# Kernel optimization log

Measured on AMD Instinct MI355X. Metric: run time of the kernel, lower is better.

The kernel has to match this reference:

```python
import jax, jax.numpy as jnp
import numpy as np

N = 50000      # nodes
F = 128        # feature_dim
H = 128        # hidden_dim
E = 1_600_000  # edges
G = 64         # graphs in batch
A = 8          # n_actions


def setup_inputs() -> dict:
    key = jax.random.key(0)
    ks = jax.random.split(key, 12)
    s = 0.05
    return {
        "x": jax.random.normal(ks[0], (N, F), jnp.float32),
        "edge_attr": jax.random.uniform(ks[1], (E, 1), jnp.float32),
        "W_e1": jax.random.normal(ks[2], (3, 1), jnp.float32) * s,
        "b_e1": jnp.zeros((1,), jnp.float32),
        "W_e2": jax.random.normal(ks[3], (1, 1), jnp.float32) * s,
        "b_e2": jnp.zeros((1,), jnp.float32),
        "W_gcn": jax.random.normal(ks[4], (F, H), jnp.float32) * s,
        "b_gcn": jnp.zeros((H,), jnp.float32),
        "W2": jax.random.normal(ks[5], (H, H), jnp.float32) * s,
        "b2": jnp.zeros((H,), jnp.float32),
        "W3": jax.random.normal(ks[6], (H, A), jnp.float32) * s,
        "b3": jnp.zeros((A,), jnp.float32),
        "edge_index": jax.random.randint(ks[7], (2, E), 0, N, jnp.int64),
        "batch": jnp.sort(jax.random.randint(ks[8], (N,), 0, G, jnp.int64)),
    }


def reference(x, edge_attr, W_e1, b_e1, W_e2, b_e2, W_gcn, b_gcn, W2, b2, W3, b3, edge_index, batch):
    # edge MLP: input is [src, dst, edge_attr] per edge -> (E, 3)
    e_feat = jnp.concatenate([edge_index.T.astype(x.dtype), edge_attr], axis=1)
    h = jax.nn.relu(e_feat @ W_e1 + b_e1)
    w = jax.nn.sigmoid(h @ W_e2 + b_e2)[:, 0]  # (E,)

    # GCNConv: add self-loops (weight 1), symmetric normalization
    loop = jnp.arange(N)
    row = jnp.concatenate([edge_index[0], loop])      # source
    col = jnp.concatenate([edge_index[1], loop])      # target
    w_all = jnp.concatenate([w, jnp.ones((N,), w.dtype)])
    deg = jax.ops.segment_sum(w_all, col, num_segments=N)
    safe_deg = jnp.where(deg > 0, deg, 1.0)
    dis = jnp.where(deg > 0, 1.0 / jnp.sqrt(safe_deg), 0.0)  # deg^-1/2, inf->0
    norm = dis[row] * w_all * dis[col]                # (E+N,)

    xw = x @ W_gcn                                    # (N, H)
    msg = norm[:, None] * xw[row]                     # (E+N, H) gather
    conv = jax.ops.segment_sum(msg, col, num_segments=N) + b_gcn  # scatter
    h1 = jax.nn.relu(conv)

    # global_mean_pool over batch index
    sums = jax.ops.segment_sum(h1, batch, num_segments=G)
    cnt = jax.ops.segment_sum(jnp.ones((N,), h1.dtype), batch, num_segments=G)
    pooled = sums / jnp.maximum(cnt, 1.0)[:, None]    # (G, H)

    h2 = jax.nn.relu(pooled @ W2 + b2)
    return h2 @ W3 + b3                               # (G, A)
```

## Files before the change

### kernel.cpp

```cpp
#include <hip/hip_runtime.h>
#include <hip/hip_fp16.h>
#include <math.h>

#define GB 64
#define AD 8
#define NC2 256
#define BSH 6
#define BS  64
#define NBMAX 1024

typedef _Float16 half8 __attribute__((ext_vector_type(8)));
typedef float    f32x4 __attribute__((ext_vector_type(4)));

__global__ __launch_bounds__(512) void k_hist2(const int* __restrict__ ei,
                                               int* __restrict__ H2,
                                               int E, int ce, int NB) {
    __shared__ int h[NBMAX];
    int c = blockIdx.x;
    for (int b = threadIdx.x; b < NB; b += 512) h[b] = 0;
    __syncthreads();
    int e0 = c * ce, e1 = min(e0 + ce, E);
    int nv = (e1 - e0) & ~3;
    const int4* dst4 = (const int4*)(ei + E + e0);
    for (int v = threadIdx.x; v < (nv >> 2); v += 512) {
        int4 d = dst4[v];
        atomicAdd(&h[d.x >> BSH], 1);
        atomicAdd(&h[d.y >> BSH], 1);
        atomicAdd(&h[d.z >> BSH], 1);
        atomicAdd(&h[d.w >> BSH], 1);
    }
    for (int e = e0 + nv + threadIdx.x; e < e1; e += 512)
        atomicAdd(&h[ei[E + e] >> BSH], 1);
    __syncthreads();
    for (int b = threadIdx.x; b < NB; b += 512)
        H2[(size_t)c * NB + b] = h[b];
}

__global__ __launch_bounds__(256) void k_cscan(int* __restrict__ H2,
                                               int* __restrict__ cntB,
                                               int NB, int nc) {
    __shared__ int ssum[256];
    int b = blockIdx.x;
    int t = threadIdx.x;
    int v = (t < nc) ? H2[(size_t)t * NB + b] : 0;
    ssum[t] = v;
    __syncthreads();
    for (int s = 1; s < 256; s <<= 1) {
        int tmp = (t >= s) ? ssum[t - s] : 0;
        __syncthreads();
        ssum[t] += tmp;
        __syncthreads();
    }
    if (t < nc) H2[(size_t)t * NB + b] = ssum[t] - v;
    if (t == 255) cntB[b] = ssum[255];
}

__global__ __launch_bounds__(1024) void k_bscan(const int* __restrict__ cntB,
                                                int* __restrict__ bb,
                                                int* __restrict__ rowptr,
                                                float* __restrict__ psum,
                                                int NB, int n, int E) {
    __shared__ int sm[1024];
    int t = threadIdx.x;
    for (int z = t; z < GB * 128 + GB; z += 1024) psum[z] = 0.0f;
    int v = (t < NB) ? cntB[t] : 0;
    sm[t] = v;
    __syncthreads();
    for (int s = 1; s < 1024; s <<= 1) {
        int tmp = (t >= s) ? sm[t - s] : 0;
        __syncthreads();
        sm[t] += tmp;
        __syncthreads();
    }
    if (t < NB) bb[t] = sm[t] - v;
    if (t == NB - 1) bb[NB] = sm[t];
    if (t == 0) rowptr[n] = E;
}

__global__ __launch_bounds__(512) void k_fill2(const int* __restrict__ ei,
                                               const float* __restrict__ attr,
                                               const float* __restrict__ W_e1,
                                               const float* __restrict__ b_e1,
                                               const float* __restrict__ W_e2,
                                               const float* __restrict__ b_e2,
                                               const int* __restrict__ bb,
                                               const int* __restrict__ H2,
                                               int2* __restrict__ rec,
                                               int E, int ce, int NB) {
    __shared__ int off[NBMAX];
    int c = blockIdx.x;
    for (int b = threadIdx.x; b < NB; b += 512)
        off[b] = bb[b] + H2[(size_t)c * NB + b];
    __syncthreads();
    float w1s = W_e1[0], w1d = W_e1[1], w1a = W_e1[2], bb1 = b_e1[0];
    float w2 = W_e2[0], bb2 = b_e2[0];
    int e0 = c * ce, e1 = min(e0 + ce, E);
    int nv = (e1 - e0) & ~3;
    const int4*   src4 = (const int4*)(ei + e0);
    const int4*   dst4 = (const int4*)(ei + E + e0);
    const float4* att4 = (const float4*)(attr + e0);
    for (int v = threadIdx.x; v < (nv >> 2); v += 512) {
        int4 sv = src4[v];
        int4 dv = dst4[v];
        float4 av = att4[v];
        int   ss[4] = {sv.x, sv.y, sv.z, sv.w};
        int   dd[4] = {dv.x, dv.y, dv.z, dv.w};
        float aa[4] = {av.x, av.y, av.z, av.w};
        #pragma unroll
        for (int k = 0; k < 4; k++) {
            float h = fmaxf((float)ss[k] * w1s + (float)dd[k] * w1d + aa[k] * w1a + bb1, 0.0f);
            float w = 1.0f / (1.0f + expf(-(h * w2 + bb2)));
            int pos = atomicAdd(&off[dd[k] >> BSH], 1);
            int2 rv;
            rv.x = ss[k] | ((dd[k] & (BS - 1)) << 16);
            rv.y = __float_as_int(w);
            rec[pos] = rv;
        }
    }
    for (int e = e0 + nv + threadIdx.x; e < e1; e += 512) {
        int d = ei[E + e];
        int s = ei[e];
        float h = fmaxf((float)s * w1s + (float)d * w1d + attr[e] * w1a + bb1, 0.0f);
        float w = 1.0f / (1.0f + expf(-(h * w2 + bb2)));
        int pos = atomicAdd(&off[d >> BSH], 1);
        int2 rv;
        rv.x = s | ((d & (BS - 1)) << 16);
        rv.y = __float_as_int(w);
        rec[pos] = rv;
    }
}

__global__ __launch_bounds__(256) void k_bucket(const int2* __restrict__ rec,
                                                const int* __restrict__ bb,
                                                unsigned int* __restrict__ rec3,
                                                int* __restrict__ rowptr,
                                                float* __restrict__ dis, int n) {
    __shared__ int   cntL[BS];
    __shared__ float degL[BS];
    __shared__ int   pfx[BS];
    __shared__ int   cnt2[BS];
    int b = blockIdx.x;
    int t = threadIdx.x;
    if (t < BS) { cntL[t] = 0; degL[t] = 1.0f; cnt2[t] = 0; }
    __syncthreads();
    int s0 = bb[b], s1 = bb[b + 1];
    for (int j = s0 + t; j < s1; j += 256) {
        int2 rv = rec[j];
        int dl = (rv.x >> 16) & (BS - 1);
        atomicAdd(&cntL[dl], 1);
        atomicAdd(&degL[dl], __int_as_float(rv.y));
    }
    __syncthreads();
    if (t == 0) {
        int acc = 0;
        for (int k = 0; k < BS; k++) { pfx[k] = acc; acc += cntL[k]; }
    }
    __syncthreads();
    int lo = b << BSH;
    if (t < BS) {
        int i = lo + t;
        if (i < n) {
            rowptr[i] = s0 + pfx[t];
            dis[i] = rsqrtf(degL[t]);
        }
    }
    for (int j = s0 + t; j < s1; j += 256) {
        int2 rv = rec[j];
        int dl = (rv.x >> 16) & (BS - 1);
        int r = atomicAdd(&cnt2[dl], 1);
        unsigned int hh = (unsigned int)__half_as_ushort(
                              __float2half(__int_as_float(rv.y)));
        rec3[s0 + pfx[dl] + r] = (unsigned int)(rv.x & 0xFFFF) | (hh << 16);
    }
}

__global__ __launch_bounds__(256) void k_xw(const float* __restrict__ x,
                                            const float* __restrict__ Wg,
                                            const float* __restrict__ dis,
                                            __half* __restrict__ xwh, int n) {
    __shared__ _Float16 Wh[128 * 136];
    int tid = threadIdx.x;
    for (int idx = tid; idx < 128 * 128; idx += 256) {
        int k = idx >> 7, c = idx & 127;
        Wh[c * 136 + k] = (_Float16)Wg[idx];
    }
    __syncthreads();

    int lane = tid & 63;
    int w = tid >> 6;
    int n16 = lane & 15;
    int quad = lane >> 4;

    #pragma unroll
    for (int hf = 0; hf < 2; hf++) {
        int r0 = blockIdx.x * 128 + hf * 64 + w * 16;
        if (r0 >= n) break;
        int arow = min(r0 + n16, n - 1);
        const float* xrow = x + (size_t)arow * 128;

        f32x4 acc[8];
        #pragma unroll
        for (int nt = 0; nt < 8; nt++) acc[nt] = (f32x4){0.f, 0.f, 0.f, 0.f};

        #pragma unroll
        for (int kk = 0; kk < 4; kk++) {
            int k0 = kk * 32 + quad * 8;
            float4 f0 = *(const float4*)(xrow + k0);
            float4 f1 = *(const float4*)(xrow + k0 + 4);
            half8 a;
            a[0] = (_Float16)f0.x; a[1] = (_Float16)f0.y;
            a[2] = (_Float16)f0.z; a[3] = (_Float16)f0.w;
            a[4] = (_Float16)f1.x; a[5] = (_Float16)f1.y;
            a[6] = (_Float16)f1.z; a[7] = (_Float16)f1.w;
            #pragma unroll
            for (int nt = 0; nt < 8; nt++) {
                half8 b = *(const half8*)&Wh[(nt * 16 + n16) * 136 + k0];
                acc[nt] = __builtin_amdgcn_mfma_f32_16x16x32_f16(a, b, acc[nt], 0, 0, 0);
            }
        }

        #pragma unroll
        for (int r = 0; r < 4; r++) {
            int row = r0 + quad * 4 + r;
            if (row < n) {
                float dv = dis[row];
                #pragma unroll
                for (int nt = 0; nt < 8; nt++)
                    xwh[(size_t)row * 128 + nt * 16 + n16] = __float2half(acc[nt][r] * dv);
            }
        }
    }
}

__global__ __launch_bounds__(256) void k_gather(const unsigned int* __restrict__ rec3,
                                                const int* __restrict__ rowptr,
                                                const float* __restrict__ dis,
                                                const __half* __restrict__ xh,
                                                const float* __restrict__ bg,
                                                __half* __restrict__ conv, int n) {
    int wave = threadIdx.x >> 6;
    int lane = threadIdx.x & 63;
    int g = lane >> 4;
    int q = lane & 15;
    int i = blockIdx.x * 4 + wave;
    if (i >= n) return;
    int st = rowptr[i];
    int m = rowptr[i + 1] - st;
    float di = dis[i];
    float acc[8];
    {
        uint4 sr = *(const uint4*)(xh + (size_t)i * 128 + q * 8);
        const __half2* hp = (const __half2*)&sr;
        float sc = (g == 0) ? 1.0f : 0.0f;
        #pragma unroll
        for (int k = 0; k < 4; k++) {
            float2 f = __half22float2(hp[k]);
            acc[2 * k]     = sc * f.x;
            acc[2 * k + 1] = sc * f.y;
        }
    }
    for (int base = 0; base < m; base += 64) {
        int kk = min(64, m - base);
        unsigned int rv = 0u;
        if (lane < kk) rv = rec3[st + base + lane];
        int jn = (kk + 3) >> 2;
        #pragma unroll 8
        for (int j = 0; j < jn; j++) {
            unsigned int rvj = (unsigned int)__builtin_amdgcn_ds_bpermute(
                                   ((j << 2) + g) << 2, (int)rv);
            int s = rvj & 0xFFFF;
            float cf = __half2float(__ushort_as_half((unsigned short)(rvj >> 16)));
            uint4 rw = *(const uint4*)(xh + (size_t)s * 128 + q * 8);
            const __half2* rp = (const __half2*)&rw;
            #pragma unroll
            for (int k = 0; k < 4; k++) {
                float2 f = __half22float2(rp[k]);
                acc[2 * k]     += cf * f.x;
                acc[2 * k + 1] += cf * f.y;
            }
        }
    }
    #pragma unroll
    for (int k = 0; k < 8; k++) {
        acc[k] += __shfl_xor(acc[k], 16);
        acc[k] += __shfl_xor(acc[k], 32);
    }
    if (g == 0) {
        float4 b0 = *(const float4*)(bg + q * 8);
        float4 b1 = *(const float4*)(bg + q * 8 + 4);
        const float* bp = (const float*)&b0;
        float v[8];
        #pragma unroll
        for (int k = 0; k < 4; k++) v[k] = fmaxf(di * acc[k] + bp[k], 0.0f);
        bp = (const float*)&b1;
        #pragma unroll
        for (int k = 0; k < 4; k++) v[4 + k] = fmaxf(di * acc[4 + k] + bp[k], 0.0f);
        __half2 h[4];
        #pragma unroll
        for (int k = 0; k < 4; k++)
            h[k] = __halves2half2(__float2half(v[2 * k]), __float2half(v[2 * k + 1]));
        uint4 o;
        o.x = *(unsigned int*)&h[0];
        o.y = *(unsigned int*)&h[1];
        o.z = *(unsigned int*)&h[2];
        o.w = *(unsigned int*)&h[3];
        *(uint4*)(conv + (size_t)i * 128 + q * 8) = o;
    }
}

__device__ __forceinline__ int lbound(const int* __restrict__ a, int n, int v) {
    int lo = 0, hi = n;
    while (lo < hi) {
        int mid = (lo + hi) >> 1;
        if (a[mid] < v) lo = mid + 1; else hi = mid;
    }
    return lo;
}

__global__ __launch_bounds__(256) void k_pool(const __half* __restrict__ h1,
                                              const int* __restrict__ batch,
                                              float* __restrict__ psum,
                                              float* __restrict__ pcnt, int n) {
    int g = blockIdx.x, ch = blockIdx.y;
    int t = threadIdx.x;
    int s = lbound(batch, n, g);
    int e = lbound(batch, n, g + 1);
    int rq = t >> 6, q = t & 63;
    float ax = 0.0f, ay = 0.0f;
    for (int i = s + ch * 4 + rq; i < e; i += 16) {
        __half2 hv = *(const __half2*)(h1 + (size_t)i * 128 + 2 * q);
        float2 f = __half22float2(hv);
        ax += f.x; ay += f.y;
    }
    __shared__ float2 sm[256];
    sm[t] = make_float2(ax, ay);
    __syncthreads();
    if (t < 64) {
        float2 a0 = sm[t], a1 = sm[t + 64], a2 = sm[t + 128], a3 = sm[t + 192];
        atomicAdd(&psum[g * 128 + 2 * q],     a0.x + a1.x + a2.x + a3.x);
        atomicAdd(&psum[g * 128 + 2 * q + 1], a0.y + a1.y + a2.y + a3.y);
    }
    if (ch == 0 && t == 0) pcnt[g] = (float)(e - s);
}

__global__ __launch_bounds__(128) void k_head(const float* __restrict__ psum,
                                              const float* __restrict__ pcnt,
                                              const float* __restrict__ W2,
                                              const float* __restrict__ b2,
                                              const float* __restrict__ W3,
                                              const float* __restrict__ b3,
                                              float* __restrict__ out) {
    __shared__ float pl[128];
    __shared__ float h2s[128];
    int g = blockIdx.x;
    int t = threadIdx.x;
    float c = fmaxf(pcnt[g], 1.0f);
    pl[t] = psum[g * 128 + t] / c;
    __syncthreads();
    float acc = b2[t];
    for (int k = 0; k < 128; k++) acc += pl[k] * W2[k * 128 + t];
    h2s[t] = fmaxf(acc, 0.0f);
    __syncthreads();
    if (t < AD) {
        float o = b3[t];
        for (int k = 0; k < 128; k++) o += h2s[k] * W3[k * AD + t];
        out[g * AD + t] = o;
    }
}

extern "C" void kernel_launch(void* const* d_in, const int* in_sizes, int n_in,
                              void* d_out, int out_size, void* d_ws, size_t ws_size,
                              hipStream_t stream) {
    const float* x        = (const float*)d_in[0];
    const float* edge_attr= (const float*)d_in[1];
    const float* W_e1     = (const float*)d_in[2];
    const float* b_e1     = (const float*)d_in[3];
    const float* W_e2     = (const float*)d_in[4];
    const float* b_e2     = (const float*)d_in[5];
    const float* W_gcn    = (const float*)d_in[6];
    const float* b_gcn    = (const float*)d_in[7];
    const float* W2       = (const float*)d_in[8];
    const float* b2       = (const float*)d_in[9];
    const float* W3       = (const float*)d_in[10];
    const float* b3       = (const float*)d_in[11];
    const int*   ei       = (const int*)d_in[12];
    const int*   batch    = (const int*)d_in[13];
    float* out = (float*)d_out;

    const int E  = in_sizes[12] / 2;
    const int n  = in_sizes[13];
    const int NB = (n + BS - 1) >> BSH;
    const int ce = (((E + NC2 - 1) / NC2) + 3) & ~3;

    char* p = (char*)d_ws;
    __half* xwh   = (__half*)p;  p += (size_t)n * 128 * sizeof(__half);
    int*    H2    = (int*)p;
    __half* conv  = (__half*)p;  p += (size_t)n * 128 * sizeof(__half);
    int2*   rec   = (int2*)p;    p += (size_t)E * sizeof(int2);
    unsigned int* rec3 = (unsigned int*)p; p += (size_t)E * sizeof(unsigned int);
    float*  dis   = (float*)p;   p += (size_t)n * sizeof(float);
    float*  psum  = (float*)p;   p += (size_t)GB * 128 * sizeof(float);
    float*  pcnt  = (float*)p;   p += (size_t)GB * sizeof(float);
    int*    rowptr= (int*)p;     p += (size_t)(n + 1) * sizeof(int);
    int*    cntB  = (int*)p;     p += (size_t)NBMAX * sizeof(int);
    int*    bb    = (int*)p;     p += (size_t)(NBMAX + 1) * sizeof(int);

    k_hist2<<<NC2, 512, 0, stream>>>(ei, H2, E, ce, NB);
    k_cscan<<<NB, 256, 0, stream>>>(H2, cntB, NB, NC2);
    k_bscan<<<1, 1024, 0, stream>>>(cntB, bb, rowptr, psum, NB, n, E);
    k_fill2<<<NC2, 512, 0, stream>>>(ei, edge_attr, W_e1, b_e1, W_e2, b_e2,
                                     bb, H2, rec, E, ce, NB);
    k_bucket<<<NB, 256, 0, stream>>>(rec, bb, rec3, rowptr, dis, n);
    k_xw<<<(n + 127) / 128, 256, 0, stream>>>(x, W_gcn, dis, xwh, n);
    k_gather<<<(n + 3) / 4, 256, 0, stream>>>(rec3, rowptr, dis, xwh,
                                              b_gcn, conv, n);
    k_pool<<<dim3(GB, 4), 256, 0, stream>>>(conv, batch, psum, pcnt, n);
    k_head<<<GB, 128, 0, stream>>>(psum, pcnt, W2, b2, W3, b3, out);
}
```

Baseline: 235.3 us.

## Split xw into four 32-feature planes and gather one plane per grid slice

After: 295.6 us. +25.6%, slower.

```diff
diff --git a/kernel.cpp b/kernel.cpp
--- a/kernel.cpp
+++ b/kernel.cpp
@@ -11,6 +11,7 @@
 
 typedef _Float16 half8 __attribute__((ext_vector_type(8)));
 typedef float    f32x4 __attribute__((ext_vector_type(4)));
+typedef unsigned int u32x4 __attribute__((ext_vector_type(4)));
 
 __global__ __launch_bounds__(512) void k_hist2(const int* __restrict__ ei,
                                                int* __restrict__ H2,
@@ -177,7 +178,7 @@
 __global__ __launch_bounds__(256) void k_xw(const float* __restrict__ x,
                                             const float* __restrict__ Wg,
                                             const float* __restrict__ dis,
-                                            __half* __restrict__ xwh, int n) {
+                                            __half* __restrict__ xwp, int n) {
     __shared__ _Float16 Wh[128 * 136];
     int tid = threadIdx.x;
     for (int idx = tid; idx < 128 * 128; idx += 256) {
@@ -225,8 +226,11 @@
             if (row < n) {
                 float dv = dis[row];
                 #pragma unroll
-                for (int nt = 0; nt < 8; nt++)
-                    xwh[(size_t)row * 128 + nt * 16 + n16] = __float2half(acc[nt][r] * dv);
+                for (int nt = 0; nt < 8; nt++) {
+                    int c = nt * 16 + n16;
+                    xwp[(size_t)(c >> 5) * n * 32 + (size_t)row * 32 + (c & 31)] =
+                        __float2half(acc[nt][r] * dv);
+                }
             }
         }
     }
@@ -235,21 +239,23 @@
 __global__ __launch_bounds__(256) void k_gather(const unsigned int* __restrict__ rec3,
                                                 const int* __restrict__ rowptr,
                                                 const float* __restrict__ dis,
-                                                const __half* __restrict__ xh,
+                                                const __half* __restrict__ xwp,
                                                 const float* __restrict__ bg,
                                                 __half* __restrict__ conv, int n) {
     int wave = threadIdx.x >> 6;
     int lane = threadIdx.x & 63;
-    int g = lane >> 4;
-    int q = lane & 15;
+    int g = lane >> 2;
+    int q = lane & 3;
+    int p = blockIdx.y;
     int i = blockIdx.x * 4 + wave;
     if (i >= n) return;
+    const __half* plane = xwp + (size_t)p * n * 32;
     int st = rowptr[i];
     int m = rowptr[i + 1] - st;
     float di = dis[i];
     float acc[8];
     {
-        uint4 sr = *(const uint4*)(xh + (size_t)i * 128 + q * 8);
+        u32x4 sr = *(const u32x4*)(plane + (size_t)i * 32 + q * 8);
         const __half2* hp = (const __half2*)&sr;
         float sc = (g == 0) ? 1.0f : 0.0f;
         #pragma unroll
@@ -262,15 +268,16 @@
     for (int base = 0; base < m; base += 64) {
         int kk = min(64, m - base);
         unsigned int rv = 0u;
-        if (lane < kk) rv = rec3[st + base + lane];
-        int jn = (kk + 3) >> 2;
-        #pragma unroll 8
+        if (lane < kk)
+            rv = __builtin_nontemporal_load(rec3 + st + base + lane);
+        int jn = (kk + 15) >> 4;
+        #pragma unroll 4
         for (int j = 0; j < jn; j++) {
             unsigned int rvj = (unsigned int)__builtin_amdgcn_ds_bpermute(
-                                   ((j << 2) + g) << 2, (int)rv);
+                                   ((j << 4) + g) << 2, (int)rv);
             int s = rvj & 0xFFFF;
             float cf = __half2float(__ushort_as_half((unsigned short)(rvj >> 16)));
-            uint4 rw = *(const uint4*)(xh + (size_t)s * 128 + q * 8);
+            u32x4 rw = *(const u32x4*)(plane + (size_t)s * 32 + q * 8);
             const __half2* rp = (const __half2*)&rw;
             #pragma unroll
             for (int k = 0; k < 4; k++) {
@@ -282,12 +289,15 @@
     }
     #pragma unroll
     for (int k = 0; k < 8; k++) {
+        acc[k] += __shfl_xor(acc[k], 4);
+        acc[k] += __shfl_xor(acc[k], 8);
         acc[k] += __shfl_xor(acc[k], 16);
         acc[k] += __shfl_xor(acc[k], 32);
     }
     if (g == 0) {
-        float4 b0 = *(const float4*)(bg + q * 8);
-        float4 b1 = *(const float4*)(bg + q * 8 + 4);
+        int f0 = p * 32 + q * 8;
+        float4 b0 = *(const float4*)(bg + f0);
+        float4 b1 = *(const float4*)(bg + f0 + 4);
         const float* bp = (const float*)&b0;
         float v[8];
         #pragma unroll
@@ -299,12 +309,12 @@
         #pragma unroll
         for (int k = 0; k < 4; k++)
             h[k] = __halves2half2(__float2half(v[2 * k]), __float2half(v[2 * k + 1]));
-        uint4 o;
+        u32x4 o;
         o.x = *(unsigned int*)&h[0];
         o.y = *(unsigned int*)&h[1];
         o.z = *(unsigned int*)&h[2];
         o.w = *(unsigned int*)&h[3];
-        *(uint4*)(conv + (size_t)i * 128 + q * 8) = o;
+        __builtin_nontemporal_store(o, (u32x4*)(conv + (size_t)i * 128 + f0));
     }
 }
 
@@ -393,7 +403,7 @@
     const int ce = (((E + NC2 - 1) / NC2) + 3) & ~3;
 
     char* p = (char*)d_ws;
-    __half* xwh   = (__half*)p;  p += (size_t)n * 128 * sizeof(__half);
+    __half* xwp   = (__half*)p;  p += (size_t)n * 128 * sizeof(__half);
     int*    H2    = (int*)p;
     __half* conv  = (__half*)p;  p += (size_t)n * 128 * sizeof(__half);
     int2*   rec   = (int2*)p;    p += (size_t)E * sizeof(int2);
@@ -411,9 +421,9 @@
     k_fill2<<<NC2, 512, 0, stream>>>(ei, edge_attr, W_e1, b_e1, W_e2, b_e2,
                                      bb, H2, rec, E, ce, NB);
     k_bucket<<<NB, 256, 0, stream>>>(rec, bb, rec3, rowptr, dis, n);
-    k_xw<<<(n + 127) / 128, 256, 0, stream>>>(x, W_gcn, dis, xwh, n);
-    k_gather<<<(n + 3) / 4, 256, 0, stream>>>(rec3, rowptr, dis, xwh,
-                                              b_gcn, conv, n);
+    k_xw<<<(n + 127) / 128, 256, 0, stream>>>(x, W_gcn, dis, xwp, n);
+    k_gather<<<dim3((n + 3) / 4, 4), 256, 0, stream>>>(rec3, rowptr, dis, xwp,
+                                                       b_gcn, conv, n);
     k_pool<<<dim3(GB, 4), 256, 0, stream>>>(conv, batch, psum, pcnt, n);
     k_head<<<GB, 128, 0, stream>>>(psum, pcnt, W2, b2, W3, b3, out);
 }
```

## Stage bucket records in LDS and use nontemporal loads/stores in gather

Applied to the files above, without the earlier changes.

Measured after the change: 237.2 us. Within noise of the previous version (+0.8%).

```diff
diff --git a/kernel.cpp b/kernel.cpp
--- a/kernel.cpp
+++ b/kernel.cpp
@@ -8,9 +8,11 @@
 #define BSH 6
 #define BS  64
 #define NBMAX 1024
+#define CAP 3072
 
 typedef _Float16 half8 __attribute__((ext_vector_type(8)));
 typedef float    f32x4 __attribute__((ext_vector_type(4)));
+typedef unsigned int u32x4 __attribute__((ext_vector_type(4)));
 
 __global__ __launch_bounds__(512) void k_hist2(const int* __restrict__ ei,
                                                int* __restrict__ H2,
@@ -135,6 +137,8 @@
                                                 unsigned int* __restrict__ rec3,
                                                 int* __restrict__ rowptr,
                                                 float* __restrict__ dis, int n) {
+    __shared__ int2  sr[CAP];
+    __shared__ unsigned int outp[CAP];
     __shared__ int   cntL[BS];
     __shared__ float degL[BS];
     __shared__ int   pfx[BS];
@@ -144,33 +148,69 @@
     if (t < BS) { cntL[t] = 0; degL[t] = 1.0f; cnt2[t] = 0; }
     __syncthreads();
     int s0 = bb[b], s1 = bb[b + 1];
-    for (int j = s0 + t; j < s1; j += 256) {
-        int2 rv = rec[j];
-        int dl = (rv.x >> 16) & (BS - 1);
-        atomicAdd(&cntL[dl], 1);
-        atomicAdd(&degL[dl], __int_as_float(rv.y));
-    }
-    __syncthreads();
-    if (t == 0) {
-        int acc = 0;
-        for (int k = 0; k < BS; k++) { pfx[k] = acc; acc += cntL[k]; }
-    }
-    __syncthreads();
-    int lo = b << BSH;
-    if (t < BS) {
-        int i = lo + t;
-        if (i < n) {
-            rowptr[i] = s0 + pfx[t];
-            dis[i] = rsqrtf(degL[t]);
-        }
-    }
-    for (int j = s0 + t; j < s1; j += 256) {
-        int2 rv = rec[j];
-        int dl = (rv.x >> 16) & (BS - 1);
-        int r = atomicAdd(&cnt2[dl], 1);
-        unsigned int hh = (unsigned int)__half_as_ushort(
-                              __float2half(__int_as_float(rv.y)));
-        rec3[s0 + pfx[dl] + r] = (unsigned int)(rv.x & 0xFFFF) | (hh << 16);
+    int m = s1 - s0;
+    if (m <= CAP) {
+        for (int j = t; j < m; j += 256) {
+            int2 rv = rec[s0 + j];
+            sr[j] = rv;
+            int dl = (rv.x >> 16) & (BS - 1);
+            atomicAdd(&cntL[dl], 1);
+            atomicAdd(&degL[dl], __int_as_float(rv.y));
+        }
+        __syncthreads();
+        if (t == 0) {
+            int acc = 0;
+            for (int k = 0; k < BS; k++) { pfx[k] = acc; acc += cntL[k]; }
+        }
+        __syncthreads();
+        int lo = b << BSH;
+        if (t < BS) {
+            int i = lo + t;
+            if (i < n) {
+                rowptr[i] = s0 + pfx[t];
+                dis[i] = rsqrtf(degL[t]);
+            }
+        }
+        for (int j = t; j < m; j += 256) {
+            int2 rv = sr[j];
+            int dl = (rv.x >> 16) & (BS - 1);
+            int r = atomicAdd(&cnt2[dl], 1);
+            unsigned int hh = (unsigned int)__half_as_ushort(
+                                  __float2half(__int_as_float(rv.y)));
+            outp[pfx[dl] + r] = (unsigned int)(rv.x & 0xFFFF) | (hh << 16);
+        }
+        __syncthreads();
+        for (int j = t; j < m; j += 256)
+            rec3[s0 + j] = outp[j];
+    } else {
+        for (int j = s0 + t; j < s1; j += 256) {
+            int2 rv = rec[j];
+            int dl = (rv.x >> 16) & (BS - 1);
+            atomicAdd(&cntL[dl], 1);
+            atomicAdd(&degL[dl], __int_as_float(rv.y));
+        }
+        __syncthreads();
+        if (t == 0) {
+            int acc = 0;
+            for (int k = 0; k < BS; k++) { pfx[k] = acc; acc += cntL[k]; }
+        }
+        __syncthreads();
+        int lo = b << BSH;
+        if (t < BS) {
+            int i = lo + t;
+            if (i < n) {
+                rowptr[i] = s0 + pfx[t];
+                dis[i] = rsqrtf(degL[t]);
+            }
+        }
+        for (int j = s0 + t; j < s1; j += 256) {
+            int2 rv = rec[j];
+            int dl = (rv.x >> 16) & (BS - 1);
+            int r = atomicAdd(&cnt2[dl], 1);
+            unsigned int hh = (unsigned int)__half_as_ushort(
+                                  __float2half(__int_as_float(rv.y)));
+            rec3[s0 + pfx[dl] + r] = (unsigned int)(rv.x & 0xFFFF) | (hh << 16);
+        }
     }
 }
 
@@ -249,7 +289,7 @@
     float di = dis[i];
     float acc[8];
     {
-        uint4 sr = *(const uint4*)(xh + (size_t)i * 128 + q * 8);
+        u32x4 sr = *(const u32x4*)(xh + (size_t)i * 128 + q * 8);
         const __half2* hp = (const __half2*)&sr;
         float sc = (g == 0) ? 1.0f : 0.0f;
         #pragma unroll
@@ -262,7 +302,8 @@
     for (int base = 0; base < m; base += 64) {
         int kk = min(64, m - base);
         unsigned int rv = 0u;
-        if (lane < kk) rv = rec3[st + base + lane];
+        if (lane < kk)
+            rv = __builtin_nontemporal_load(rec3 + st + base + lane);
         int jn = (kk + 3) >> 2;
         #pragma unroll 8
         for (int j = 0; j < jn; j++) {
@@ -270,7 +311,7 @@
                                    ((j << 2) + g) << 2, (int)rv);
             int s = rvj & 0xFFFF;
             float cf = __half2float(__ushort_as_half((unsigned short)(rvj >> 16)));
-            uint4 rw = *(const uint4*)(xh + (size_t)s * 128 + q * 8);
+            u32x4 rw = *(const u32x4*)(xh + (size_t)s * 128 + q * 8);
             const __half2* rp = (const __half2*)&rw;
             #pragma unroll
             for (int k = 0; k < 4; k++) {
@@ -299,12 +340,12 @@
         #pragma unroll
         for (int k = 0; k < 4; k++)
             h[k] = __halves2half2(__float2half(v[2 * k]), __float2half(v[2 * k + 1]));
-        uint4 o;
+        u32x4 o;
         o.x = *(unsigned int*)&h[0];
         o.y = *(unsigned int*)&h[1];
         o.z = *(unsigned int*)&h[2];
         o.w = *(unsigned int*)&h[3];
-        *(uint4*)(conv + (size_t)i * 128 + q * 8) = o;
+        __builtin_nontemporal_store(o, (u32x4*)(conv + (size_t)i * 128 + q * 8));
     }
 }
 
```

## Fuse bucket-local sort, gather and mean-pool into one per-bucket kernel

Applied to the files above, without the earlier changes.

Result: slower. 253.3 us (+7.7%).

```diff
diff --git a/kernel.cpp b/kernel.cpp
--- a/kernel.cpp
+++ b/kernel.cpp
@@ -8,9 +8,12 @@
 #define BSH 6
 #define BS  64
 #define NBMAX 1024
+#define CAP 3072
+#define GSPAN 4
 
 typedef _Float16 half8 __attribute__((ext_vector_type(8)));
 typedef float    f32x4 __attribute__((ext_vector_type(4)));
+typedef unsigned int u32x4 __attribute__((ext_vector_type(4)));
 
 __global__ __launch_bounds__(512) void k_hist2(const int* __restrict__ ei,
                                                int* __restrict__ H2,
@@ -62,7 +65,7 @@
                                                 int NB, int n, int E) {
     __shared__ int sm[1024];
     int t = threadIdx.x;
-    for (int z = t; z < GB * 128 + GB; z += 1024) psum[z] = 0.0f;
+    for (int z = t; z < GB * 128; z += 1024) psum[z] = 0.0f;
     int v = (t < NB) ? cntB[t] : 0;
     sm[t] = v;
     __syncthreads();
@@ -130,18 +133,16 @@
     }
 }
 
-__global__ __launch_bounds__(256) void k_bucket(const int2* __restrict__ rec,
-                                                const int* __restrict__ bb,
-                                                unsigned int* __restrict__ rec3,
-                                                int* __restrict__ rowptr,
-                                                float* __restrict__ dis, int n) {
+__global__ __launch_bounds__(256) void k_deg(const int2* __restrict__ rec,
+                                             const int* __restrict__ bb,
+                                             int* __restrict__ rowptr,
+                                             float* __restrict__ dis, int n) {
     __shared__ int   cntL[BS];
     __shared__ float degL[BS];
     __shared__ int   pfx[BS];
-    __shared__ int   cnt2[BS];
     int b = blockIdx.x;
     int t = threadIdx.x;
-    if (t < BS) { cntL[t] = 0; degL[t] = 1.0f; cnt2[t] = 0; }
+    if (t < BS) { cntL[t] = 0; degL[t] = 1.0f; }
     __syncthreads();
     int s0 = bb[b], s1 = bb[b + 1];
     for (int j = s0 + t; j < s1; j += 256) {
@@ -163,14 +164,6 @@
             rowptr[i] = s0 + pfx[t];
             dis[i] = rsqrtf(degL[t]);
         }
-    }
-    for (int j = s0 + t; j < s1; j += 256) {
-        int2 rv = rec[j];
-        int dl = (rv.x >> 16) & (BS - 1);
-        int r = atomicAdd(&cnt2[dl], 1);
-        unsigned int hh = (unsigned int)__half_as_ushort(
-                              __float2half(__int_as_float(rv.y)));
-        rec3[s0 + pfx[dl] + r] = (unsigned int)(rv.x & 0xFFFF) | (hh << 16);
     }
 }
 
@@ -232,79 +225,135 @@
     }
 }
 
-__global__ __launch_bounds__(256) void k_gather(const unsigned int* __restrict__ rec3,
+__global__ __launch_bounds__(512) void k_gather(const int2* __restrict__ rec,
+                                                const int* __restrict__ bb,
                                                 const int* __restrict__ rowptr,
                                                 const float* __restrict__ dis,
+                                                const int* __restrict__ batch,
                                                 const __half* __restrict__ xh,
                                                 const float* __restrict__ bg,
-                                                __half* __restrict__ conv, int n) {
-    int wave = threadIdx.x >> 6;
-    int lane = threadIdx.x & 63;
+                                                float* __restrict__ psum, int n) {
+    __shared__ unsigned int outL[CAP];
+    __shared__ float psumL[GSPAN * 128];
+    __shared__ int   rowL[BS];
+    __shared__ int   cntL[BS];
+    __shared__ int   batchL[BS];
+    __shared__ float disL[BS];
+    int b = blockIdx.x;
+    int t = threadIdx.x;
+    int lo = b << BSH;
+    int s0 = bb[b], s1 = bb[b + 1];
+    int m_all = s1 - s0;
+    if (t < GSPAN * 128) psumL[t] = 0.0f;
+    if (t < BS) {
+        int i = lo + t;
+        cntL[t] = 0;
+        if (i < n) {
+            rowL[t] = rowptr[i] - s0;
+            batchL[t] = batch[i];
+            disL[t] = dis[i];
+        } else {
+            rowL[t] = m_all; batchL[t] = -1; disL[t] = 0.0f;
+        }
+    }
+    __syncthreads();
+    int gb0 = batchL[0];
+    int hiN = min(lo + BS - 1, n - 1);
+    int span = batch[hiN] - gb0 + 1;
+
+    bool fast = (m_all <= CAP);
+    if (fast) {
+        for (int j = t; j < m_all; j += 512) {
+            int2 rv = rec[s0 + j];
+            int dl = (rv.x >> 16) & (BS - 1);
+            int r = atomicAdd(&cntL[dl], 1);
+            unsigned int hh = (unsigned int)__half_as_ushort(
+                                  __float2half(__int_as_float(rv.y)));
+            outL[rowL[dl] + r] = (unsigned int)(rv.x & 0xFFFF) | (hh << 16);
+        }
+    }
+    __syncthreads();
+
+    int wave = t >> 6;
+    int lane = t & 63;
     int g = lane >> 4;
     int q = lane & 15;
-    int i = blockIdx.x * 4 + wave;
-    if (i >= n) return;
-    int st = rowptr[i];
-    int m = rowptr[i + 1] - st;
-    float di = dis[i];
-    float acc[8];
-    {
-        uint4 sr = *(const uint4*)(xh + (size_t)i * 128 + q * 8);
-        const __half2* hp = (const __half2*)&sr;
-        float sc = (g == 0) ? 1.0f : 0.0f;
+    for (int k = 0; k < 8; k++) {
+        int dl = wave * 8 + k;
+        int i = lo + dl;
+        if (i >= n) break;
+        int st = rowL[dl];
+        int m = cntL[dl];
+        float di = disL[dl];
+        float acc[8];
+        {
+            u32x4 sr = *(const u32x4*)(xh + (size_t)i * 128 + q * 8);
+            const __half2* hp = (const __half2*)&sr;
+            float sc = (g == 0) ? 1.0f : 0.0f;
+            #pragma unroll
+            for (int kk = 0; kk < 4; kk++) {
+                float2 f = __half22float2(hp[kk]);
+                acc[2 * kk]     = sc * f.x;
+                acc[2 * kk + 1] = sc * f.y;
+            }
+        }
+        if (fast) {
+            #pragma unroll 4
+            for (int j = g; j < m; j += 4) {
+                unsigned int u = outL[st + j];
+                int s = u & 0xFFFF;
+                float cf = __half2float(__ushort_as_half((unsigned short)(u >> 16)));
+                u32x4 rw = *(const u32x4*)(xh + (size_t)s * 128 + q * 8);
+                const __half2* rp = (const __half2*)&rw;
+                #pragma unroll
+                for (int kk = 0; kk < 4; kk++) {
+                    float2 f = __half22float2(rp[kk]);
+                    acc[2 * kk]     += cf * f.x;
+                    acc[2 * kk + 1] += cf * f.y;
+                }
+            }
+        } else {
+            for (int j = g; j < m_all; j += 4) {
+                int2 rv = rec[s0 + j];
+                if (((rv.x >> 16) & (BS - 1)) == dl) {
+                    float cf = __int_as_float(rv.y);
+                    int s = rv.x & 0xFFFF;
+                    u32x4 rw = *(const u32x4*)(xh + (size_t)s * 128 + q * 8);
+                    const __half2* rp = (const __half2*)&rw;
+                    #pragma unroll
+                    for (int kk = 0; kk < 4; kk++) {
+                        float2 f = __half22float2(rp[kk]);
+                        acc[2 * kk]     += cf * f.x;
+                        acc[2 * kk + 1] += cf * f.y;
+                    }
+                }
+            }
+        }
         #pragma unroll
-        for (int k = 0; k < 4; k++) {
-            float2 f = __half22float2(hp[k]);
-            acc[2 * k]     = sc * f.x;
-            acc[2 * k + 1] = sc * f.y;
-        }
-    }
-    for (int base = 0; base < m; base += 64) {
-        int kk = min(64, m - base);
-        unsigned int rv = 0u;
-        if (lane < kk) rv = rec3[st + base + lane];
-        int jn = (kk + 3) >> 2;
-        #pragma unroll 8
-        for (int j = 0; j < jn; j++) {
-            unsigned int rvj = (unsigned int)__builtin_amdgcn_ds_bpermute(
-                                   ((j << 2) + g) << 2, (int)rv);
-            int s = rvj & 0xFFFF;
-            float cf = __half2float(__ushort_as_half((unsigned short)(rvj >> 16)));
-            uint4 rw = *(const uint4*)(xh + (size_t)s * 128 + q * 8);
-            const __half2* rp = (const __half2*)&rw;
+        for (int kk = 0; kk < 8; kk++) {
+            acc[kk] += __shfl_xor(acc[kk], 16);
+            acc[kk] += __shfl_xor(acc[kk], 32);
+        }
+        if (g == 0) {
+            int gi = batchL[dl] - gb0;
             #pragma unroll
-            for (int k = 0; k < 4; k++) {
-                float2 f = __half22float2(rp[k]);
-                acc[2 * k]     += cf * f.x;
-                acc[2 * k + 1] += cf * f.y;
-            }
-        }
-    }
-    #pragma unroll
-    for (int k = 0; k < 8; k++) {
-        acc[k] += __shfl_xor(acc[k], 16);
-        acc[k] += __shfl_xor(acc[k], 32);
-    }
-    if (g == 0) {
-        float4 b0 = *(const float4*)(bg + q * 8);
-        float4 b1 = *(const float4*)(bg + q * 8 + 4);
-        const float* bp = (const float*)&b0;
-        float v[8];
-        #pragma unroll
-        for (int k = 0; k < 4; k++) v[k] = fmaxf(di * acc[k] + bp[k], 0.0f);
-        bp = (const float*)&b1;
-        #pragma unroll
-        for (int k = 0; k < 4; k++) v[4 + k] = fmaxf(di * acc[4 + k] + bp[k], 0.0f);
-        __half2 h[4];
-        #pragma unroll
-        for (int k = 0; k < 4; k++)
-            h[k] = __halves2half2(__float2half(v[2 * k]), __float2half(v[2 * k + 1]));
-        uint4 o;
-        o.x = *(unsigned int*)&h[0];
-        o.y = *(unsigned int*)&h[1];
-        o.z = *(unsigned int*)&h[2];
-        o.w = *(unsigned int*)&h[3];
-        *(uint4*)(conv + (size_t)i * 128 + q * 8) = o;
+            for (int kk = 0; kk < 8; kk++) {
+                float v = fmaxf(di * acc[kk] + bg[q * 8 + kk], 0.0f);
+                if (span <= GSPAN)
+                    atomicAdd(&psumL[gi * 128 + q * 8 + kk], v);
+                else
+                    atomicAdd(&psum[batchL[dl] * 128 + q * 8 + kk], v);
+            }
+        }
+    }
+    __syncthreads();
+    if (span <= GSPAN) {
+        int tot = span * 128;
+        for (int idx = t; idx < tot; idx += 512) {
+            float v = psumL[idx];
+            if (v != 0.0f)
+                atomicAdd(&psum[(gb0 + (idx >> 7)) * 128 + (idx & 127)], v);
+        }
     }
 }
 
@@ -317,44 +366,20 @@
     return lo;
 }
 
-__global__ __launch_bounds__(256) void k_pool(const __half* __restrict__ h1,
+__global__ __launch_bounds__(128) void k_head(const float* __restrict__ psum,
                                               const int* __restrict__ batch,
-                                              float* __restrict__ psum,
-                                              float* __restrict__ pcnt, int n) {
-    int g = blockIdx.x, ch = blockIdx.y;
-    int t = threadIdx.x;
-    int s = lbound(batch, n, g);
-    int e = lbound(batch, n, g + 1);
-    int rq = t >> 6, q = t & 63;
-    float ax = 0.0f, ay = 0.0f;
-    for (int i = s + ch * 4 + rq; i < e; i += 16) {
-        __half2 hv = *(const __half2*)(h1 + (size_t)i * 128 + 2 * q);
-        float2 f = __half22float2(hv);
-        ax += f.x; ay += f.y;
-    }
-    __shared__ float2 sm[256];
-    sm[t] = make_float2(ax, ay);
-    __syncthreads();
-    if (t < 64) {
-        float2 a0 = sm[t], a1 = sm[t + 64], a2 = sm[t + 128], a3 = sm[t + 192];
-        atomicAdd(&psum[g * 128 + 2 * q],     a0.x + a1.x + a2.x + a3.x);
-        atomicAdd(&psum[g * 128 + 2 * q + 1], a0.y + a1.y + a2.y + a3.y);
-    }
-    if (ch == 0 && t == 0) pcnt[g] = (float)(e - s);
-}
-
-__global__ __launch_bounds__(128) void k_head(const float* __restrict__ psum,
-                                              const float* __restrict__ pcnt,
                                               const float* __restrict__ W2,
                                               const float* __restrict__ b2,
                                               const float* __restrict__ W3,
                                               const float* __restrict__ b3,
-                                              float* __restrict__ out) {
+                                              float* __restrict__ out, int n) {
     __shared__ float pl[128];
     __shared__ float h2s[128];
     int g = blockIdx.x;
     int t = threadIdx.x;
-    float c = fmaxf(pcnt[g], 1.0f);
+    int s = lbound(batch, n, g);
+    int e = lbound(batch, n, g + 1);
+    float c = fmaxf((float)(e - s), 1.0f);
     pl[t] = psum[g * 128 + t] / c;
     __syncthreads();
     float acc = b2[t];
@@ -394,13 +419,10 @@
 
     char* p = (char*)d_ws;
     __half* xwh   = (__half*)p;  p += (size_t)n * 128 * sizeof(__half);
-    int*    H2    = (int*)p;
-    __half* conv  = (__half*)p;  p += (size_t)n * 128 * sizeof(__half);
+    int*    H2    = (int*)p;     p += (size_t)NC2 * NB * sizeof(int);
     int2*   rec   = (int2*)p;    p += (size_t)E * sizeof(int2);
-    unsigned int* rec3 = (unsigned int*)p; p += (size_t)E * sizeof(unsigned int);
     float*  dis   = (float*)p;   p += (size_t)n * sizeof(float);
     float*  psum  = (float*)p;   p += (size_t)GB * 128 * sizeof(float);
-    float*  pcnt  = (float*)p;   p += (size_t)GB * sizeof(float);
     int*    rowptr= (int*)p;     p += (size_t)(n + 1) * sizeof(int);
     int*    cntB  = (int*)p;     p += (size_t)NBMAX * sizeof(int);
     int*    bb    = (int*)p;     p += (size_t)(NBMAX + 1) * sizeof(int);
@@ -410,10 +432,9 @@
     k_bscan<<<1, 1024, 0, stream>>>(cntB, bb, rowptr, psum, NB, n, E);
     k_fill2<<<NC2, 512, 0, stream>>>(ei, edge_attr, W_e1, b_e1, W_e2, b_e2,
                                      bb, H2, rec, E, ce, NB);
-    k_bucket<<<NB, 256, 0, stream>>>(rec, bb, rec3, rowptr, dis, n);
+    k_deg<<<NB, 256, 0, stream>>>(rec, bb, rowptr, dis, n);
     k_xw<<<(n + 127) / 128, 256, 0, stream>>>(x, W_gcn, dis, xwh, n);
-    k_gather<<<(n + 3) / 4, 256, 0, stream>>>(rec3, rowptr, dis, xwh,
-                                              b_gcn, conv, n);
-    k_pool<<<dim3(GB, 4), 256, 0, stream>>>(conv, batch, psum, pcnt, n);
-    k_head<<<GB, 128, 0, stream>>>(psum, pcnt, W2, b2, W3, b3, out);
-}
+    k_gather<<<NB, 512, 0, stream>>>(rec, bb, rowptr, dis, batch, xwh,
+                                     b_gcn, psum, n);
+    k_head<<<GB, 128, 0, stream>>>(psum, batch, W2, b2, W3, b3, out, n);
+}
```
